# Performance work log

Hardware: AMD Instinct MI355X
Metric: run time of the kernel (lower is better)

## Reference

```python
import jax, jax.numpy as jnp
import numpy as np

B, S, HID = 4, 1024, 1024
NH = 16
DH = HID // NH  # 64


def _split_heads(t):
    # [B, S, HID] -> [B, NH, S, DH]
    return t.reshape(B, S, NH, DH).transpose(0, 2, 1, 3)


def _merge_heads(t):
    # [B, NH, S, DH] -> [B, S, HID]
    return t.transpose(0, 2, 1, 3).reshape(B, S, HID)


def setup_inputs() -> dict:
    key = jax.random.key(0)
    ks = jax.random.split(key, 13)
    scale = 1.0 / np.sqrt(HID)
    inp = {"x": jax.random.normal(ks[0], (B, S, HID), dtype=jnp.float32)}
    names = ["Wq", "Wk", "Wv", "Wq2", "Wk2", "Wv2"]
    for i, n in enumerate(names):
        inp[n] = jax.random.normal(ks[1 + i], (HID, HID), dtype=jnp.float32) * scale
        inp["b" + n[1:]] = jax.random.normal(ks[7 + i], (HID,), dtype=jnp.float32) * 0.01
    return inp


def _attn(q, k, v):
    # q,k,v: [B, NH, S, DH]
    scores = jnp.einsum("bhqd,bhkd->bhqk", q, k) / np.sqrt(DH).astype(np.float32)
    probs = jax.nn.softmax(scores, axis=-1)
    return jnp.einsum("bhqk,bhkd->bhqd", probs, v)


def reference(x, Wq, bq, Wk, bk, Wv, bv, Wq2, bq2, Wk2, bk2, Wv2, bv2):
    # nn.Linear: y = x @ W.T + b
    q1 = _split_heads(x @ Wq.T + bq)
    k1 = _split_heads(x @ Wk.T + bk)
    v1 = _split_heads(x @ Wv.T + bv)
    q2 = _split_heads(x @ Wq2.T + bq2)
    k2 = _split_heads(x @ Wk2.T + bk2)
    v2 = _split_heads(x @ Wv2.T + bv2)
    # 5'UTR direction: q1 attends to k2/v2; 3'UTR direction: q2 attends to k1/v1
    out5 = _merge_heads(_attn(q1, k2, v2))
    out3 = _merge_heads(_attn(q2, k1, v1))
    return (out5, out3)
```

## Files before the change

kernel.cpp:

```cpp
#include <hip/hip_runtime.h>


typedef __attribute__((ext_vector_type(8))) short bf16x8;
typedef __attribute__((ext_vector_type(4))) short bf16x4;
typedef __attribute__((ext_vector_type(4))) float f32x4;
typedef __attribute__((ext_vector_type(4))) short s16x4;

#define MFMA16(a, b, c) __builtin_amdgcn_mfma_f32_16x16x32_bf16(a, b, c, 0, 0, 0)
#define BARRIER() asm volatile("s_barrier" ::: "memory")
#define VMCNT0() asm volatile("s_waitcnt vmcnt(0)" ::: "memory")

__device__ __forceinline__ f32x4 mfma16k(bf16x4 a, bf16x4 b, f32x4 c) {
#if __has_builtin(__builtin_amdgcn_mfma_f32_16x16x16bf16_1k)
  return __builtin_amdgcn_mfma_f32_16x16x16bf16_1k(a, b, c, 0, 0, 0);
#elif __has_builtin(__builtin_amdgcn_mfma_f32_16x16x16_bf16)
  return __builtin_amdgcn_mfma_f32_16x16x16_bf16(a, b, c, 0, 0, 0);
#else
  asm volatile("v_mfma_f32_16x16x16_bf16 %0, %1, %2, %0"
               : "+v"(c) : "v"(a), "v"(b));
  return c;
#endif
}

__device__ __forceinline__ unsigned short f2bf(float f) {
  unsigned u = __float_as_uint(f);
  u = (u + 0x7fffu + ((u >> 16) & 1u)) >> 16;
  return (unsigned short)u;
}

__device__ __forceinline__ unsigned cvt_pk_bf16(float lo, float hi) {
  unsigned r;
  asm("v_cvt_pk_bf16_f32 %0, %1, %2" : "=v"(r) : "v"(lo), "v"(hi));
  return r;
}

__device__ __forceinline__ void gll16(const void* g, void* l) {
  __builtin_amdgcn_global_load_lds(
      (const __attribute__((address_space(1))) unsigned int*)g,
      (__attribute__((address_space(3))) unsigned int*)l, 16, 0, 0);
}

__global__ __launch_bounds__(256) void convert_k(
    const float* __restrict__ x,
    const float* __restrict__ W0, const float* __restrict__ W1,
    const float* __restrict__ W2, const float* __restrict__ W3,
    const float* __restrict__ W4, const float* __restrict__ W5,
    short* __restrict__ xbf, short* __restrict__ wbf) {
  const int total = (10 << 20) >> 2;
  for (int tid = blockIdx.x * 256 + threadIdx.x; tid < total;
       tid += 2048 * 256) {
    const int e = tid << 2;
    const float* src;
    short* dst;
    int off;
    if (e < (4 << 20)) {
      src = x; dst = xbf; off = e;
    } else {
      const int j = e - (4 << 20);
      const int wsel = j >> 20;
      off = j & ((1 << 20) - 1);
      src = (wsel == 0) ? W0 : (wsel == 1) ? W1 : (wsel == 2) ? W2
          : (wsel == 3) ? W3 : (wsel == 4) ? W4 : W5;
      dst = wbf + ((size_t)wsel << 20);
    }
    const float4 v = *(const float4*)(src + off);
    s16x4 o;
    o.x = (short)f2bf(v.x);
    o.y = (short)f2bf(v.y);
    o.z = (short)f2bf(v.z);
    o.w = (short)f2bf(v.w);
    *(s16x4*)(dst + off) = o;
  }
}

__global__ __launch_bounds__(256, 2) void proj_t2(
    const short* __restrict__ Ag, const short* __restrict__ Wall,
    const float* __restrict__ bq, const float* __restrict__ bk,
    const float* __restrict__ bv, const float* __restrict__ bq2,
    const float* __restrict__ bk2, const float* __restrict__ bv2,
    short* __restrict__ qkv) {
  __shared__ __align__(16) short As[2][8192];
  __shared__ __align__(16) short Bs[2][12288];

  const int bid = blockIdx.x;
  const int xcd = bid & 7, i = bid >> 3;
  const int ns = i & 3, mb = i >> 2;
  const int nbase = (xcd * 4 + ns) * 192;
  const int m0 = mb << 7;

  const int t = threadIdx.x, lane = t & 63, w = t >> 6;
  const int g = lane >> 4, lr = lane & 15;
  const int wr = w >> 1, wc = w & 1;

  f32x4 acc[4][6] = {};

  auto stage_a = [&](int T) {
#pragma unroll
    for (int ld = 0; ld < 4; ++ld) {
      const int slot = (ld << 8) + t;
      const int rr = slot >> 3;
      const int gc = (slot & 7) ^ (rr & 7);
      gll16(Ag + (size_t)(m0 + rr) * 1024 + (T << 6) + (gc << 3),
            &As[T & 1][slot * 8]);
    }
  };
  auto stage_b = [&](int T) {
#pragma unroll
    for (int ld = 0; ld < 6; ++ld) {
      const int slot = (ld << 8) + t;
      const int rr = slot >> 3;
      const int gc = (slot & 7) ^ (rr & 7);
      gll16(Wall + (size_t)(nbase + rr) * 1024 + (T << 6) + (gc << 3),
            &Bs[T & 1][slot * 8]);
    }
  };

  stage_a(0); stage_b(0);
  VMCNT0();
  BARRIER();

#define LOAD_A(KK, TB)                                                    \
  _Pragma("unroll") for (int mi = 0; mi < 4; ++mi) {                      \
    const int rA = wr * 64 + mi * 16 + lr;                                \
    af[mi] = *(const bf16x8*)                                             \
        &As[TB][rA * 64 + ((((KK) * 4 + g) ^ (rA & 7)) << 3)];            \
  }
#define LOAD_B(KK, TB)                                                    \
  _Pragma("unroll") for (int nj = 0; nj < 6; ++nj) {                      \
    const int rB = wc * 96 + nj * 16 + lr;                                \
    bf[nj] = *(const bf16x8*)                                             \
        &Bs[TB][rB * 64 + ((((KK) * 4 + g) ^ (rB & 7)) << 3)];            \
  }
#define MFMA_C()                                                          \
  __builtin_amdgcn_s_setprio(1);                                          \
  _Pragma("unroll") for (int mi = 0; mi < 4; ++mi)                        \
    _Pragma("unroll") for (int nj = 0; nj < 6; ++nj)                      \
      acc[mi][nj] = MFMA16(af[mi], bf[nj], acc[mi][nj]);                  \
  __builtin_amdgcn_s_setprio(0);

  for (int T = 0; T < 16; ++T) {
    const int C = T & 1;
    const bool DV = T < 15;
    bf16x8 af[4], bf[6];
    {
      LOAD_A(0, C); LOAD_B(0, C);
      if (DV) stage_a(T + 1);
      BARRIER();
      MFMA_C();
      BARRIER();
    }
    {
      LOAD_A(1, C); LOAD_B(1, C);
      if (DV) stage_b(T + 1);
      BARRIER();
      MFMA_C();
      VMCNT0();
      BARRIER();
    }
  }

#undef LOAD_A
#undef LOAD_B
#undef MFMA_C

#pragma unroll
  for (int nj = 0; nj < 6; ++nj) {
    const int nn = nbase + wc * 96 + nj * 16 + lr;
    const int p = nn >> 10, nl = nn & 1023;
    const float* bp = (p == 0) ? bq : (p == 1) ? bk : (p == 2) ? bv
                    : (p == 3) ? bq2 : (p == 4) ? bk2 : bv2;
    const float bb = bp[nl];
    const int h = nl >> 6, d = nl & 63;
    const int pt = (p == 0 || p == 3) ? 0 : (p == 1 || p == 4) ? 1 : 2;
    unsigned short* dst = (unsigned short*)qkv + ((size_t)p << 22);
#pragma unroll
    for (int mi = 0; mi < 4; ++mi) {
#pragma unroll
      for (int r = 0; r < 4; ++r) {
        const int m = m0 + wr * 64 + mi * 16 + (g << 2) + r;
        const int b = m >> 10, s = m & 1023;
        const unsigned short val = f2bf(acc[mi][nj][r] + bb);
        size_t idx;
        if (pt == 0) {
          idx = ((size_t)(((b << 4) + h) * 1024 + s) << 6) + d;
        } else if (pt == 1) {
          const int d2 = (d & 7) | (((d >> 3) ^ (s & 7)) << 3);
          idx = ((size_t)(((b << 4) + h) * 1024 + s) << 6) + d2;
        } else {
          const int tt = s >> 6, s2 = s & 63;
          const int w2 = (s2 & 7) ^ (((d >> 3) & 1) << 2);
          const int s3 = w2 | (((s2 >> 3) ^ (d & 7)) << 3);
          idx = ((size_t)((((b << 4) + h) * 16 + tt) * 64 + d) << 6) + s3;
        }
        dst[idx] = val;
      }
    }
  }
}

__global__ __launch_bounds__(512) void attn_k(const short* __restrict__ qkv,
                                              float* __restrict__ out) {
  __shared__ __align__(16) short Ks[2][64 * 64];
  __shared__ __align__(16) short Vs[2][64 * 64];

  const int L = blockIdx.x;
  const int xcd = L & 7, ss = L >> 3;
  const int qt = ss & 7, pg = ss >> 3;
  const int pp = xcd + (pg << 3);
  const int hb = pp & 63, dir = pp >> 6;

  const short* Q = qkv + ((size_t)(dir ? 3 : 0) << 22) + ((size_t)hb << 16);
  const short* K = qkv + ((size_t)(dir ? 1 : 4) << 22) + ((size_t)hb << 16);
  const short* V = qkv + ((size_t)(dir ? 2 : 5) << 22) + ((size_t)hb << 16);
  float* O = out + ((size_t)dir << 22);

  const int t = threadIdx.x, lane = t & 63, w = t >> 6;
  const int g = lane >> 4, lr = lane & 15;

  const int qrow = (qt << 7) + (w << 4) + lr;
  bf16x8 qf[2];
  qf[0] = *(const bf16x8*)(Q + qrow * 64 + g * 8);
  qf[1] = *(const bf16x8*)(Q + qrow * 64 + 32 + g * 8);

  const bf16x4 ones4 = {0x3F80, 0x3F80, 0x3F80, 0x3F80};

  f32x4 oacc[4] = {};
  f32x4 lacc = {};
  float mrun = -3.0e38f;
  const float CSC = 0.18033688f;

  const int srow = t >> 3;
  const int scol = (t & 7) << 3;

  auto stage = [&](int kt, int buf) {
    gll16(K + (size_t)((kt << 6) + srow) * 64 + scol, &Ks[buf][w << 9]);
    gll16(V + (size_t)(kt << 12) + (size_t)srow * 64 + scol, &Vs[buf][w << 9]);
  };

  auto tile = [&](int kt, auto curc) {
    constexpr int CUR = decltype(curc)::value;
    if (kt < 15) stage(kt + 1, CUR ^ 1);

    f32x4 sc2[4] = {};
    __builtin_amdgcn_s_setprio(1);
#pragma unroll
    for (int dk = 0; dk < 2; ++dk) {
#pragma unroll
      for (int kn = 0; kn < 4; ++kn) {
        const int krow = kn * 16 + lr;
        const bf16x8 kf = *(const bf16x8*)
            &Ks[CUR][krow * 64 +
                     ((((dk << 6) + (g << 4)) ^ ((krow & 7) << 4)) >> 1)];
        sc2[kn] = MFMA16(kf, qf[dk], sc2[kn]);
      }
    }
    __builtin_amdgcn_s_setprio(0);

    float tm = fmaxf(fmaxf(fmaxf(sc2[0][0], sc2[0][1]),
                           fmaxf(sc2[0][2], sc2[0][3])),
                     fmaxf(fmaxf(sc2[1][0], sc2[1][1]),
                           fmaxf(sc2[1][2], sc2[1][3])));
    tm = fmaxf(tm, fmaxf(fmaxf(fmaxf(sc2[2][0], sc2[2][1]),
                               fmaxf(sc2[2][2], sc2[2][3])),
                         fmaxf(fmaxf(sc2[3][0], sc2[3][1]),
                               fmaxf(sc2[3][2], sc2[3][3]))));
    const bool ok = __all(fmaf(tm, CSC, -mrun) <= 8.0f);
    if (!ok) {
      float t2 = fmaxf(tm, __shfl_xor(tm, 16));
      t2 = fmaxf(t2, __shfl_xor(t2, 32));
      const float mnew = fmaxf(mrun, t2 * CSC);
      const float scq = exp2f(mrun - mnew);
      mrun = mnew;
#pragma unroll
      for (int r = 0; r < 4; ++r) {
        const float sr = __shfl(scq, (g << 2) + r);
        lacc[r] *= sr;
#pragma unroll
        for (int dn = 0; dn < 4; ++dn) oacc[dn][r] *= sr;
      }
    }

    bf16x4 pa[4];
#pragma unroll
    for (int kn = 0; kn < 4; ++kn) {
      const float p0 = exp2f(fmaf(sc2[kn][0], CSC, -mrun));
      const float p1 = exp2f(fmaf(sc2[kn][1], CSC, -mrun));
      const float p2 = exp2f(fmaf(sc2[kn][2], CSC, -mrun));
      const float p3 = exp2f(fmaf(sc2[kn][3], CSC, -mrun));
      union { unsigned u[2]; bf16x4 v; } pk;
      pk.u[0] = cvt_pk_bf16(p0, p1);
      pk.u[1] = cvt_pk_bf16(p2, p3);
      pa[kn] = pk.v;
    }

    __builtin_amdgcn_s_setprio(1);
#pragma unroll
    for (int kn = 0; kn < 4; ++kn) {
      lacc = mfma16k(pa[kn], ones4, lacc);
#pragma unroll
      for (int dn = 0; dn < 4; ++dn) {
        const int vrow = dn * 16 + lr;
        const int ch = (2 * kn + (g >> 1)) ^ (vrow & 7);
        const int sub = (((g & 1) ^ ((lr >> 3) & 1)) << 2);
        const bf16x4 vf = *(const bf16x4*)
            &Vs[CUR][vrow * 64 + ch * 8 + sub];
        oacc[dn] = mfma16k(pa[kn], vf, oacc[dn]);
      }
    }
    __builtin_amdgcn_s_setprio(0);

    VMCNT0();
    BARRIER();
  };

  stage(0, 0);
  VMCNT0();
  BARRIER();

#pragma unroll
  for (int kp = 0; kp < 8; ++kp) {
    tile(2 * kp, std::integral_constant<int, 0>{});
    tile(2 * kp + 1, std::integral_constant<int, 1>{});
  }

  const int b = hb >> 4, h = hb & 15;
  float rl[4];
#pragma unroll
  for (int r = 0; r < 4; ++r) rl[r] = 1.0f / lacc[r];
#pragma unroll
  for (int dn = 0; dn < 4; ++dn) {
#pragma unroll
    for (int r = 0; r < 4; ++r) {
      const int q = (qt << 7) + (w << 4) + (g << 2) + r;
      const int d = dn * 16 + lr;
      O[((size_t)(b * 1024 + q) << 10) + h * 64 + d] = oacc[dn][r] * rl[r];
    }
  }
}

extern "C" void kernel_launch(void* const* d_in, const int* in_sizes, int n_in,
                              void* d_out, int out_size, void* d_ws,
                              size_t ws_size, hipStream_t stream) {
  const float* x   = (const float*)d_in[0];
  const float* Wq  = (const float*)d_in[1];
  const float* bq  = (const float*)d_in[2];
  const float* Wk  = (const float*)d_in[3];
  const float* bk  = (const float*)d_in[4];
  const float* Wv  = (const float*)d_in[5];
  const float* bv  = (const float*)d_in[6];
  const float* Wq2 = (const float*)d_in[7];
  const float* bq2 = (const float*)d_in[8];
  const float* Wk2 = (const float*)d_in[9];
  const float* bk2 = (const float*)d_in[10];
  const float* Wv2 = (const float*)d_in[11];
  const float* bv2 = (const float*)d_in[12];

  char* ws = (char*)d_ws;
  short* xbf = (short*)ws;
  short* wbf = (short*)(ws + 8388608);
  short* qkv = (short*)(ws + 20971520);

  convert_k<<<2048, 256, 0, stream>>>(x, Wq, Wk, Wv, Wq2, Wk2, Wv2, xbf, wbf);
  proj_t2<<<1024, 256, 0, stream>>>(xbf, wbf, bq, bk, bv, bq2, bk2,
                                    bv2, qkv);
  attn_k<<<1024, 512, 0, stream>>>(qkv, (float*)d_out);
}
```

Before: 144.7 us.

## Process two 16-row query tiles per wave to reuse K/V LDS reads

```diff
diff --git a/kernel.cpp b/kernel.cpp
--- a/kernel.cpp
+++ b/kernel.cpp
@@ -205,7 +205,7 @@
 
   const int L = blockIdx.x;
   const int xcd = L & 7, ss = L >> 3;
-  const int qt = ss & 7, pg = ss >> 3;
+  const int qt = ss & 3, pg = ss >> 2;
   const int pp = xcd + (pg << 3);
   const int hb = pp & 63, dir = pp >> 6;
 
@@ -217,16 +217,18 @@
   const int t = threadIdx.x, lane = t & 63, w = t >> 6;
   const int g = lane >> 4, lr = lane & 15;
 
-  const int qrow = (qt << 7) + (w << 4) + lr;
-  bf16x8 qf[2];
-  qf[0] = *(const bf16x8*)(Q + qrow * 64 + g * 8);
-  qf[1] = *(const bf16x8*)(Q + qrow * 64 + 32 + g * 8);
+  const int qrow = (qt << 8) + (w << 5) + lr;
+  bf16x8 qfA[2], qfB[2];
+  qfA[0] = *(const bf16x8*)(Q + qrow * 64 + g * 8);
+  qfA[1] = *(const bf16x8*)(Q + qrow * 64 + 32 + g * 8);
+  qfB[0] = *(const bf16x8*)(Q + (qrow + 16) * 64 + g * 8);
+  qfB[1] = *(const bf16x8*)(Q + (qrow + 16) * 64 + 32 + g * 8);
 
   const bf16x4 ones4 = {0x3F80, 0x3F80, 0x3F80, 0x3F80};
 
-  f32x4 oacc[4] = {};
-  f32x4 lacc = {};
-  float mrun = -3.0e38f;
+  f32x4 oaccA[4] = {}, oaccB[4] = {};
+  f32x4 laccA = {}, laccB = {};
+  float mrunA = -3.0e38f, mrunB = -3.0e38f;
   const float CSC = 0.18033688f;
 
   const int srow = t >> 3;
@@ -237,33 +239,16 @@
     gll16(V + (size_t)(kt << 12) + (size_t)srow * 64 + scol, &Vs[buf][w << 9]);
   };
 
-  auto tile = [&](int kt, auto curc) {
-    constexpr int CUR = decltype(curc)::value;
-    if (kt < 15) stage(kt + 1, CUR ^ 1);
-
-    f32x4 sc2[4] = {};
-    __builtin_amdgcn_s_setprio(1);
-#pragma unroll
-    for (int dk = 0; dk < 2; ++dk) {
-#pragma unroll
-      for (int kn = 0; kn < 4; ++kn) {
-        const int krow = kn * 16 + lr;
-        const bf16x8 kf = *(const bf16x8*)
-            &Ks[CUR][krow * 64 +
-                     ((((dk << 6) + (g << 4)) ^ ((krow & 7) << 4)) >> 1)];
-        sc2[kn] = MFMA16(kf, qf[dk], sc2[kn]);
-      }
-    }
-    __builtin_amdgcn_s_setprio(0);
-
-    float tm = fmaxf(fmaxf(fmaxf(sc2[0][0], sc2[0][1]),
-                           fmaxf(sc2[0][2], sc2[0][3])),
-                     fmaxf(fmaxf(sc2[1][0], sc2[1][1]),
-                           fmaxf(sc2[1][2], sc2[1][3])));
-    tm = fmaxf(tm, fmaxf(fmaxf(fmaxf(sc2[2][0], sc2[2][1]),
-                               fmaxf(sc2[2][2], sc2[2][3])),
-                         fmaxf(fmaxf(sc2[3][0], sc2[3][1]),
-                               fmaxf(sc2[3][2], sc2[3][3]))));
+  auto softmax = [&](f32x4* sc, float& mrun, f32x4& lacc, f32x4* oacc,
+                     bf16x4* pa) {
+    float tm = fmaxf(fmaxf(fmaxf(sc[0][0], sc[0][1]),
+                           fmaxf(sc[0][2], sc[0][3])),
+                     fmaxf(fmaxf(sc[1][0], sc[1][1]),
+                           fmaxf(sc[1][2], sc[1][3])));
+    tm = fmaxf(tm, fmaxf(fmaxf(fmaxf(sc[2][0], sc[2][1]),
+                               fmaxf(sc[2][2], sc[2][3])),
+                         fmaxf(fmaxf(sc[3][0], sc[3][1]),
+                               fmaxf(sc[3][2], sc[3][3]))));
     const bool ok = __all(fmaf(tm, CSC, -mrun) <= 8.0f);
     if (!ok) {
       float t2 = fmaxf(tm, __shfl_xor(tm, 16));
@@ -279,24 +264,48 @@
         for (int dn = 0; dn < 4; ++dn) oacc[dn][r] *= sr;
       }
     }
-
-    bf16x4 pa[4];
 #pragma unroll
     for (int kn = 0; kn < 4; ++kn) {
-      const float p0 = exp2f(fmaf(sc2[kn][0], CSC, -mrun));
-      const float p1 = exp2f(fmaf(sc2[kn][1], CSC, -mrun));
-      const float p2 = exp2f(fmaf(sc2[kn][2], CSC, -mrun));
-      const float p3 = exp2f(fmaf(sc2[kn][3], CSC, -mrun));
+      const float p0 = exp2f(fmaf(sc[kn][0], CSC, -mrun));
+      const float p1 = exp2f(fmaf(sc[kn][1], CSC, -mrun));
+      const float p2 = exp2f(fmaf(sc[kn][2], CSC, -mrun));
+      const float p3 = exp2f(fmaf(sc[kn][3], CSC, -mrun));
       union { unsigned u[2]; bf16x4 v; } pk;
       pk.u[0] = cvt_pk_bf16(p0, p1);
       pk.u[1] = cvt_pk_bf16(p2, p3);
       pa[kn] = pk.v;
     }
-
+  };
+
+  auto tile = [&](int kt, auto curc) {
+    constexpr int CUR = decltype(curc)::value;
+    if (kt < 15) stage(kt + 1, CUR ^ 1);
+
+    f32x4 scA[4] = {}, scB[4] = {};
     __builtin_amdgcn_s_setprio(1);
 #pragma unroll
+    for (int dk = 0; dk < 2; ++dk) {
+#pragma unroll
+      for (int kn = 0; kn < 4; ++kn) {
+        const int krow = kn * 16 + lr;
+        const bf16x8 kf = *(const bf16x8*)
+            &Ks[CUR][krow * 64 +
+                     ((((dk << 6) + (g << 4)) ^ ((krow & 7) << 4)) >> 1)];
+        scA[kn] = MFMA16(kf, qfA[dk], scA[kn]);
+        scB[kn] = MFMA16(kf, qfB[dk], scB[kn]);
+      }
+    }
+    __builtin_amdgcn_s_setprio(0);
+
+    bf16x4 paA[4], paB[4];
+    softmax(scA, mrunA, laccA, oaccA, paA);
+    softmax(scB, mrunB, laccB, oaccB, paB);
+
+    __builtin_amdgcn_s_setprio(1);
+#pragma unroll
     for (int kn = 0; kn < 4; ++kn) {
-      lacc = mfma16k(pa[kn], ones4, lacc);
+      laccA = mfma16k(paA[kn], ones4, laccA);
+      laccB = mfma16k(paB[kn], ones4, laccB);
 #pragma unroll
       for (int dn = 0; dn < 4; ++dn) {
         const int vrow = dn * 16 + lr;
@@ -304,7 +313,8 @@
         const int sub = (((g & 1) ^ ((lr >> 3) & 1)) << 2);
         const bf16x4 vf = *(const bf16x4*)
             &Vs[CUR][vrow * 64 + ch * 8 + sub];
-        oacc[dn] = mfma16k(pa[kn], vf, oacc[dn]);
+        oaccA[dn] = mfma16k(paA[kn], vf, oaccA[dn]);
+        oaccB[dn] = mfma16k(paB[kn], vf, oaccB[dn]);
       }
     }
     __builtin_amdgcn_s_setprio(0);
@@ -324,16 +334,21 @@
   }
 
   const int b = hb >> 4, h = hb & 15;
-  float rl[4];
-#pragma unroll
-  for (int r = 0; r < 4; ++r) rl[r] = 1.0f / lacc[r];
+  float rlA[4], rlB[4];
+#pragma unroll
+  for (int r = 0; r < 4; ++r) {
+    rlA[r] = 1.0f / laccA[r];
+    rlB[r] = 1.0f / laccB[r];
+  }
 #pragma unroll
   for (int dn = 0; dn < 4; ++dn) {
 #pragma unroll
     for (int r = 0; r < 4; ++r) {
-      const int q = (qt << 7) + (w << 4) + (g << 2) + r;
+      const int qA = (qt << 8) + (w << 5) + (g << 2) + r;
       const int d = dn * 16 + lr;
-      O[((size_t)(b * 1024 + q) << 10) + h * 64 + d] = oacc[dn][r] * rl[r];
+      O[((size_t)(b * 1024 + qA) << 10) + h * 64 + d] = oaccA[dn][r] * rlA[r];
+      O[((size_t)(b * 1024 + qA + 16) << 10) + h * 64 + d] =
+          oaccB[dn][r] * rlB[r];
     }
   }
 }
@@ -363,5 +378,5 @@
   convert_k<<<2048, 256, 0, stream>>>(x, Wq, Wk, Wv, Wq2, Wk2, Wv2, xbf, wbf);
   proj_t2<<<1024, 256, 0, stream>>>(xbf, wbf, bq, bk, bv, bq2, bk2,
                                     bv2, qkv);
-  attn_k<<<1024, 512, 0, stream>>>(qkv, (float*)d_out);
-}
+  attn_k<<<512, 512, 0, stream>>>(qkv, (float*)d_out);
+}
```

Measured after the change: 153.6 us. +6.1%, slower.
